# Kernel optimization log

Measured on AMD Instinct MI355X. Metric: run time of the kernel, lower is better.

The kernel has to match this reference:

```python
import jax, jax.numpy as jnp
import numpy as np

B, S, D, H = 2, 2048, 1024, 16
DK = D // H


def setup_inputs() -> dict:
    key = jax.random.key(0)
    ks = jax.random.split(key, 8)
    Q = jax.random.normal(ks[0], (B, S, D), dtype=jnp.float32)
    K = jax.random.normal(ks[1], (B, S, D), dtype=jnp.float32)
    V = jax.random.normal(ks[2], (B, S, D), dtype=jnp.float32)
    # causal mask (1 = keep), broadcastable to [B, H, S, S]
    mask = jnp.tril(jnp.ones((S, S), dtype=bool))[None, None, :, :]
    # xavier_uniform for [D, D]: bound = sqrt(6 / (D + D))
    bound = float(np.sqrt(6.0 / (D + D)))
    def xavier(k):
        return jax.random.uniform(k, (D, D), jnp.float32, -bound, bound)
    Wq, Wk, Wv, Wo = xavier(ks[3]), xavier(ks[4]), xavier(ks[5]), xavier(ks[6])
    bq = jnp.zeros((D,), jnp.float32)
    bk = jnp.zeros((D,), jnp.float32)
    bv = jnp.zeros((D,), jnp.float32)
    bo = jnp.zeros((D,), jnp.float32)
    return {"Q": Q, "K": K, "V": V, "mask": mask,
            "Wq": Wq, "bq": bq, "Wk": Wk, "bk": bk,
            "Wv": Wv, "bv": bv, "Wo": Wo, "bo": bo}


def _split_heads(x):
    # [B, S, D] -> [B, H, S, DK]
    b, s, _ = x.shape
    return x.reshape(b, s, H, DK).transpose(0, 2, 1, 3)


def reference(Q, K, V, mask, Wq, bq, Wk, bk, Wv, bv, Wo, bo):
    # linear projections (torch Linear: x @ W.T + b)
    q = _split_heads(Q @ Wq.T + bq)  # [B, H, S, DK]
    k = _split_heads(K @ Wk.T + bk)
    v = _split_heads(V @ Wv.T + bv)
    scale = 1.0 / jnp.sqrt(jnp.asarray(DK, q.dtype))
    scores = jnp.einsum('bhqd,bhkd->bhqk', q, k) * scale  # [B, H, S, S]
    scores = jnp.where(mask, scores, jnp.asarray(-1e9, scores.dtype))
    attn = jax.nn.softmax(scores, axis=-1)
    ctx = jnp.einsum('bhqk,bhkd->bhqd', attn, v)  # [B, H, S, DK]
    ctx = ctx.transpose(0, 2, 1, 3).reshape(Q.shape[0], Q.shape[1], D)
    out = ctx @ Wo.T + bo  # dropout is identity in eval mode
    return out, attn
```

## Files before the change

### kernel.cpp

```cpp
#include <hip/hip_runtime.h>
#include <hip/hip_bf16.h>

#define B_  2
#define S_  2048
#define D_  1024
#define H_  16
#define DK_ 64
#define M_  (B_*S_)
#define NT_ (S_/64)
#define NE_ (B_*S_*D_)
#define NW_ (D_*D_)

typedef __attribute__((ext_vector_type(8))) short short8;
typedef __attribute__((ext_vector_type(4))) float f32x4;

static __device__ __forceinline__ unsigned short f2bf(float f) {
    union { float f; unsigned u; } v; v.f = f;
    unsigned r = (v.u + 0x7fffu + ((v.u >> 16) & 1u)) >> 16;
    return (unsigned short)r;
}

static __device__ __forceinline__ void gload16(const void* g, void* l) {
    __builtin_amdgcn_global_load_lds((const __attribute__((address_space(1))) void*)g,
                                     (__attribute__((address_space(3))) void*)l, 16, 0, 0);
}

__global__ __launch_bounds__(256) void conv7(const float* __restrict__ q,  const float* __restrict__ k,
                                             const float* __restrict__ v,  const float* __restrict__ wq,
                                             const float* __restrict__ wk, const float* __restrict__ wv,
                                             const float* __restrict__ wo, unsigned short* __restrict__ ws)
{
    const float* src[7] = {q, k, v, wq, wk, wv, wo};
    const int    n4[7]  = {NE_/4, NE_/4, NE_/4, NW_/4, NW_/4, NW_/4, NW_/4};
    size_t off = 0;
    #pragma unroll
    for (int seg = 0; seg < 7; ++seg) {
        unsigned short* dst = ws + off;
        for (int i = blockIdx.x*256 + threadIdx.x; i < n4[seg]; i += gridDim.x*256) {
            float4 x = ((const float4*)src[seg])[i];
            union { unsigned short u[4]; unsigned long long ll; } cv;
            cv.u[0]=f2bf(x.x); cv.u[1]=f2bf(x.y); cv.u[2]=f2bf(x.z); cv.u[3]=f2bf(x.w);
            ((unsigned long long*)dst)[i] = cv.ll;
        }
        off += (size_t)n4[seg]*4;
    }
}

__global__ __launch_bounds__(256) void gemm_bt(const unsigned short* __restrict__ A,
                                               const unsigned short* __restrict__ Bt,
                                               const float* __restrict__ bias,
                                               void* __restrict__ outv, int out_mode)
{
    __shared__ unsigned short as_[128][64];
    __shared__ unsigned short bs_[64][64];

    const int tid  = threadIdx.x;
    const int wave = tid >> 6, lane = tid & 63;
    const int lq   = lane & 15, quad = lane >> 4;
    const int m0   = blockIdx.y * 128, n0 = blockIdx.x * 64;
    const int wm   = (wave >> 1) * 64, wn = (wave & 1) * 32;

    f32x4 acc[4][2] = {};

    for (int k0 = 0; k0 < D_; k0 += 64) {
        __syncthreads();
        #pragma unroll
        for (int i = 0; i < 4; ++i) {
            const int p = tid + i*256, row = p >> 3, c = (p & 7) ^ (row & 7);
            gload16(A + (size_t)(m0+row)*D_ + k0 + c*8,
                    (char*)as_ + (size_t)(wave*64 + i*256)*16);
        }
        #pragma unroll
        for (int i = 0; i < 2; ++i) {
            const int p = tid + i*256, row = p >> 3, c = (p & 7) ^ (row & 7);
            gload16(Bt + (size_t)(n0+row)*D_ + k0 + c*8,
                    (char*)bs_ + (size_t)(wave*64 + i*256)*16);
        }
        __syncthreads();

        #pragma unroll
        for (int kk = 0; kk < 2; ++kk) {
            short8 a[4], b[2];
            #pragma unroll
            for (int i = 0; i < 4; ++i) {
                const int row = wm + i*16 + lq;
                a[i] = *(const short8*)((const char*)as_ + row*128 + (((kk*4+quad) ^ (row&7))*16));
            }
            #pragma unroll
            for (int j = 0; j < 2; ++j) {
                const int row = wn + j*16 + lq;
                b[j] = *(const short8*)((const char*)bs_ + row*128 + (((kk*4+quad) ^ (row&7))*16));
            }
            #pragma unroll
            for (int i = 0; i < 4; ++i)
                #pragma unroll
                for (int j = 0; j < 2; ++j)
                    acc[i][j] = __builtin_amdgcn_mfma_f32_16x16x32_bf16(a[i], b[j], acc[i][j], 0, 0, 0);
        }
    }

    float bcol[2];
    #pragma unroll
    for (int j = 0; j < 2; ++j) bcol[j] = bias[n0 + wn + j*16 + lq];

    if (out_mode == 0) {
        float* out = (float*)outv;
        #pragma unroll
        for (int i = 0; i < 4; ++i)
            #pragma unroll
            for (int j = 0; j < 2; ++j) {
                const int col = n0 + wn + j*16 + lq;
                #pragma unroll
                for (int r = 0; r < 4; ++r) {
                    const int m = m0 + wm + i*16 + quad*4 + r;
                    out[(size_t)m*D_ + col] = acc[i][j][r] + bcol[j];
                }
            }
    } else {
        unsigned short* out = (unsigned short*)outv;
        #pragma unroll
        for (int i = 0; i < 4; ++i)
            #pragma unroll
            for (int j = 0; j < 2; ++j) {
                const int col = n0 + wn + j*16 + lq;
                const int h = col >> 6, dk = col & 63;
                #pragma unroll
                for (int r = 0; r < 4; ++r) {
                    const int m  = m0 + wm + i*16 + quad*4 + r;
                    const int bb = m >> 11, s = m & (S_-1);
                    out[(((size_t)(bb*H_ + h))*S_ + s)*DK_ + dk] = f2bf(acc[i][j][r] + bcol[j]);
                }
            }
    }
}

__global__ __launch_bounds__(256) void transpose_v(const unsigned short* __restrict__ vp,
                                                   unsigned short* __restrict__ vt)
{
    __shared__ unsigned short ts[64][72];
    const int tid = threadIdx.x;
    const int s0  = blockIdx.x * 64;
    const size_t bh = (size_t)blockIdx.z * H_ + blockIdx.y;
    const unsigned short* src = vp + (bh * S_ + s0) * DK_;
    #pragma unroll
    for (int i = 0; i < 2; ++i) {
        int idx = tid + i*256;
        *(short8*)&ts[idx >> 3][(idx & 7)*8] = *(const short8*)(src + idx*8);
    }
    __syncthreads();
    unsigned short* dst = vt + bh * DK_ * S_;
    #pragma unroll
    for (int i = 0; i < 2; ++i) {
        int idx = tid + i*256;
        int dk = idx >> 3, c = idx & 7;
        union { unsigned short u[8]; short8 v; } pk;
        #pragma unroll
        for (int j = 0; j < 8; ++j) pk.u[j] = ts[c*8 + j][dk];
        *(short8*)(dst + (size_t)dk*S_ + s0 + c*8) = pk.v;
    }
}

__global__ __launch_bounds__(256) void attn_mfma(const unsigned short* __restrict__ q,
                                                 const unsigned short* __restrict__ k,
                                                 const unsigned short* __restrict__ vt,
                                                 float* __restrict__ attn,
                                                 unsigned short* __restrict__ ctx)
{
    __shared__ unsigned short qs[2][64][64];
    __shared__ unsigned short ks[64][64];
    __shared__ unsigned short vts[64][64];
    __shared__ unsigned short es[4][16][72];

    const int tid  = threadIdx.x;
    const int wave = tid >> 6, lane = tid & 63;
    const int lq   = lane & 15, quad = lane >> 4;

    const int g = blockIdx.x;
    const int xcd = g & 7, i5 = g >> 3;
    const int x = i5 >> 2;
    const int bhid = xcd + 8*(i5 & 3);
    const int h = bhid & (H_-1), b = bhid >> 4;

    const int itA = x, itB = NT_-1 - x;
    const size_t bh = (size_t)(b*H_ + h);
    const unsigned short* kb  = k  + bh*S_*DK_;
    const unsigned short* vtb = vt + bh*(size_t)DK_*S_;
    const unsigned short* qbA = q + (bh*S_ + (size_t)itA*64) * DK_;
    const unsigned short* qbB = q + (bh*S_ + (size_t)itB*64) * DK_;
    float* attn_bA = attn + bh*(size_t)S_*S_ + (size_t)itA*64*S_;
    float* attn_bB = attn + bh*(size_t)S_*S_ + (size_t)itB*64*S_;

    #pragma unroll
    for (int t = 0; t < 2; ++t) {
        const unsigned short* qb = t ? qbB : qbA;
        #pragma unroll
        for (int i = 0; i < 2; ++i) {
            const int p = tid + i*256, row = p >> 3, c = (p & 7) ^ (row & 7);
            gload16(qb + (size_t)row*DK_ + c*8,
                    (char*)&qs[t][0][0] + (size_t)(wave*64 + i*256)*16);
        }
    }
    __syncthreads();

    const int wr0  = wave*16;
    const int rgA0 = itA*64 + wr0 + quad*4;
    const int rgB0 = itB*64 + wr0 + quad*4;

    short8 aA0, aA1, aB0, aB1;
    {
        const int row = wr0 + lq;
        const int s0 = ((quad)     ^ (row & 7)) * 16;
        const int s1 = ((4 + quad) ^ (row & 7)) * 16;
        aA0 = *(const short8*)((const char*)&qs[0][row][0] + s0);
        aA1 = *(const short8*)((const char*)&qs[0][row][0] + s1);
        aB0 = *(const short8*)((const char*)&qs[1][row][0] + s0);
        aB1 = *(const short8*)((const char*)&qs[1][row][0] + s1);
    }

    float rsA[4] = {0.f,0.f,0.f,0.f}, rsB[4] = {0.f,0.f,0.f,0.f};
    for (int jt = 0; jt <= itB; ++jt) {
        __syncthreads();
        #pragma unroll
        for (int i = 0; i < 2; ++i) {
            const int p = tid + i*256, row = p >> 3, c = (p & 7) ^ (row & 7);
            gload16(kb + ((size_t)jt*64 + row)*DK_ + c*8,
                    (char*)&ks[0][0] + (size_t)(wave*64 + i*256)*16);
        }
        __syncthreads();
        const int actA = (jt <= itA);
        #pragma unroll
        for (int j = 0; j < 4; ++j) {
            const int krow = j*16 + lq;
            const int s0 = ((quad)     ^ (krow & 7)) * 16;
            const int s1 = ((4 + quad) ^ (krow & 7)) * 16;
            const short8 b0 = *(const short8*)((const char*)&ks[krow][0] + s0);
            const short8 b1 = *(const short8*)((const char*)&ks[krow][0] + s1);
            const int cg = jt*64 + j*16 + lq;
            {
                f32x4 s = {};
                s = __builtin_amdgcn_mfma_f32_16x16x32_bf16(aB0, b0, s, 0, 0, 0);
                s = __builtin_amdgcn_mfma_f32_16x16x32_bf16(aB1, b1, s, 0, 0, 0);
                #pragma unroll
                for (int r = 0; r < 4; ++r)
                    if (cg <= rgB0 + r) rsB[r] += __expf(s[r]*0.125f);
            }
            if (actA) {
                f32x4 s = {};
                s = __builtin_amdgcn_mfma_f32_16x16x32_bf16(aA0, b0, s, 0, 0, 0);
                s = __builtin_amdgcn_mfma_f32_16x16x32_bf16(aA1, b1, s, 0, 0, 0);
                #pragma unroll
                for (int r = 0; r < 4; ++r)
                    if (cg <= rgA0 + r) rsA[r] += __expf(s[r]*0.125f);
            }
        }
    }
    #pragma unroll
    for (int m = 1; m < 16; m <<= 1)
        #pragma unroll
        for (int r = 0; r < 4; ++r) {
            rsA[r] += __shfl_xor(rsA[r], m, 64);
            rsB[r] += __shfl_xor(rsB[r], m, 64);
        }
    float invA[4], invB[4];
    #pragma unroll
    for (int r = 0; r < 4; ++r) { invA[r] = 1.0f/rsA[r]; invB[r] = 1.0f/rsB[r]; }

    f32x4 cA[4] = {}, cB[4] = {};
    for (int jt = 0; jt <= itB; ++jt) {
        __syncthreads();
        #pragma unroll
        for (int i = 0; i < 2; ++i) {
            const int p = tid + i*256, row = p >> 3, c = (p & 7) ^ (row & 7);
            gload16(kb + ((size_t)jt*64 + row)*DK_ + c*8,
                    (char*)&ks[0][0]  + (size_t)(wave*64 + i*256)*16);
            gload16(vtb + (size_t)row*S_ + jt*64 + c*8,
                    (char*)&vts[0][0] + (size_t)(wave*64 + i*256)*16);
        }
        __syncthreads();
        const int actA = (jt <= itA);

        #pragma unroll
        for (int j = 0; j < 4; ++j) {
            const int krow = j*16 + lq;
            const int s0 = ((quad)     ^ (krow & 7)) * 16;
            const int s1 = ((4 + quad) ^ (krow & 7)) * 16;
            const short8 b0 = *(const short8*)((const char*)&ks[krow][0] + s0);
            const short8 b1 = *(const short8*)((const char*)&ks[krow][0] + s1);
            const int cg = jt*64 + j*16 + lq;
            f32x4 s = {};
            s = __builtin_amdgcn_mfma_f32_16x16x32_bf16(aB0, b0, s, 0, 0, 0);
            s = __builtin_amdgcn_mfma_f32_16x16x32_bf16(aB1, b1, s, 0, 0, 0);
            #pragma unroll
            for (int r = 0; r < 4; ++r) {
                const float e = (cg <= rgB0 + r) ? __expf(s[r]*0.125f)*invB[r] : 0.f;
                attn_bB[(size_t)(wr0 + quad*4 + r)*S_ + cg] = e;
                es[wave][quad*4 + r][j*16 + lq] = f2bf(e);
            }
        }
        {
            const short8 p0 = *(const short8*)&es[wave][lq][quad*8];
            const short8 p1 = *(const short8*)&es[wave][lq][32 + quad*8];
            #pragma unroll
            for (int j = 0; j < 4; ++j) {
                const int vrow = j*16 + lq;
                const int s0 = ((quad)     ^ (vrow & 7)) * 16;
                const int s1 = ((4 + quad) ^ (vrow & 7)) * 16;
                cB[j] = __builtin_amdgcn_mfma_f32_16x16x32_bf16(
                    p0, *(const short8*)((const char*)&vts[vrow][0] + s0), cB[j], 0, 0, 0);
                cB[j] = __builtin_amdgcn_mfma_f32_16x16x32_bf16(
                    p1, *(const short8*)((const char*)&vts[vrow][0] + s1), cB[j], 0, 0, 0);
            }
        }

        if (actA) {
            #pragma unroll
            for (int j = 0; j < 4; ++j) {
                const int krow = j*16 + lq;
                const int s0 = ((quad)     ^ (krow & 7)) * 16;
                const int s1 = ((4 + quad) ^ (krow & 7)) * 16;
                const short8 b0 = *(const short8*)((const char*)&ks[krow][0] + s0);
                const short8 b1 = *(const short8*)((const char*)&ks[krow][0] + s1);
                const int cg = jt*64 + j*16 + lq;
                f32x4 s = {};
                s = __builtin_amdgcn_mfma_f32_16x16x32_bf16(aA0, b0, s, 0, 0, 0);
                s = __builtin_amdgcn_mfma_f32_16x16x32_bf16(aA1, b1, s, 0, 0, 0);
                #pragma unroll
                for (int r = 0; r < 4; ++r) {
                    const float e = (cg <= rgA0 + r) ? __expf(s[r]*0.125f)*invA[r] : 0.f;
                    attn_bA[(size_t)(wr0 + quad*4 + r)*S_ + cg] = e;
                    es[wave][quad*4 + r][j*16 + lq] = f2bf(e);
                }
            }
            const short8 p0 = *(const short8*)&es[wave][lq][quad*8];
            const short8 p1 = *(const short8*)&es[wave][lq][32 + quad*8];
            #pragma unroll
            for (int j = 0; j < 4; ++j) {
                const int vrow = j*16 + lq;
                const int s0 = ((quad)     ^ (vrow & 7)) * 16;
                const int s1 = ((4 + quad) ^ (vrow & 7)) * 16;
                cA[j] = __builtin_amdgcn_mfma_f32_16x16x32_bf16(
                    p0, *(const short8*)((const char*)&vts[vrow][0] + s0), cA[j], 0, 0, 0);
                cA[j] = __builtin_amdgcn_mfma_f32_16x16x32_bf16(
                    p1, *(const short8*)((const char*)&vts[vrow][0] + s1), cA[j], 0, 0, 0);
            }
        }
    }

    #pragma unroll
    for (int j = 0; j < 4; ++j) {
        const int dk = j*16 + lq;
        #pragma unroll
        for (int r = 0; r < 4; ++r) {
            const int sA = itA*64 + wr0 + quad*4 + r;
            const int sB = itB*64 + wr0 + quad*4 + r;
            ctx[((size_t)b*S_ + sA)*D_ + h*DK_ + dk] = f2bf(cA[j][r]);
            ctx[((size_t)b*S_ + sB)*D_ + h*DK_ + dk] = f2bf(cB[j][r]);
        }
    }

    const float4 z4 = make_float4(0.f, 0.f, 0.f, 0.f);
    {
        const int zc0 = (itA+1)*64;
        float* rowp = attn_bA + (size_t)(tid >> 2)*S_;
        for (int c = zc0 + (tid & 3)*4; c < S_; c += 16) *(float4*)&rowp[c] = z4;
    }
    {
        const int zc0 = (itB+1)*64;
        if (zc0 < S_) {
            float* rowp = attn_bB + (size_t)(tid >> 2)*S_;
            for (int c = zc0 + (tid & 3)*4; c < S_; c += 16) *(float4*)&rowp[c] = z4;
        }
    }
}

extern "C" void kernel_launch(void* const* d_in, const int* in_sizes, int n_in,
                              void* d_out, int out_size, void* d_ws, size_t ws_size,
                              hipStream_t stream)
{
    const float* Q  = (const float*)d_in[0];
    const float* K  = (const float*)d_in[1];
    const float* V  = (const float*)d_in[2];
    const float* Wq = (const float*)d_in[4];
    const float* bq = (const float*)d_in[5];
    const float* Wk = (const float*)d_in[6];
    const float* bk = (const float*)d_in[7];
    const float* Wv = (const float*)d_in[8];
    const float* bv = (const float*)d_in[9];
    const float* Wo = (const float*)d_in[10];
    const float* bo = (const float*)d_in[11];

    float* out  = (float*)d_out;
    float* attn = out + (size_t)B_*S_*D_;

    unsigned short* ws = (unsigned short*)d_ws;
    const size_t R  = (size_t)NE_;
    const size_t W1 = (size_t)NW_;
    unsigned short* Qb  = ws;
    unsigned short* Kb  = ws + R;
    unsigned short* Vb  = ws + 2*R;
    unsigned short* Wqb = ws + 3*R;
    unsigned short* Wkb = Wqb + W1;
    unsigned short* Wvb = Wkb + W1;
    unsigned short* Wob = Wvb + W1;
    unsigned short* qp  = Wob + W1;
    unsigned short* kp  = qp + R;
    unsigned short* vp  = kp + R;
    unsigned short* vtw = vp + R;
    unsigned short* ctx = vtw + R;

    conv7<<<2048, 256, 0, stream>>>(Q, K, V, Wq, Wk, Wv, Wo, ws);

    dim3 ggrid(D_/64, M_/128);
    gemm_bt<<<ggrid, 256, 0, stream>>>(Qb, Wqb, bq, qp, 1);
    gemm_bt<<<ggrid, 256, 0, stream>>>(Kb, Wkb, bk, kp, 1);
    gemm_bt<<<ggrid, 256, 0, stream>>>(Vb, Wvb, bv, vp, 1);
    transpose_v<<<dim3(S_/64, H_, B_), 256, 0, stream>>>(vp, vtw);
    attn_mfma<<<(NT_/2)*H_*B_, 256, 0, stream>>>(qp, kp, vtw, attn, ctx);
    gemm_bt<<<ggrid, 256, 0, stream>>>(ctx, Wob, bo, out, 0);
}
```

Measured before the change: 806.2 us.

## Double-buffer GEMM and attention tiles, batch QKV GEMMs, split attention across 8 waves

```diff
diff --git a/kernel.cpp b/kernel.cpp
--- a/kernel.cpp
+++ b/kernel.cpp
@@ -46,50 +46,62 @@
     }
 }
 
-__global__ __launch_bounds__(256) void gemm_bt(const unsigned short* __restrict__ A,
-                                               const unsigned short* __restrict__ Bt,
-                                               const float* __restrict__ bias,
+__global__ __launch_bounds__(256) void gemm_bt(const unsigned short* __restrict__ A0,
+                                               const unsigned short* __restrict__ W0,
+                                               const float* __restrict__ b0,
+                                               const float* __restrict__ b1,
+                                               const float* __restrict__ b2,
                                                void* __restrict__ outv, int out_mode)
 {
-    __shared__ unsigned short as_[128][64];
-    __shared__ unsigned short bs_[64][64];
+    __shared__ unsigned short as2[2][128][64];
+    __shared__ unsigned short bs2[2][64][64];
 
     const int tid  = threadIdx.x;
-    const int wave = tid >> 6, lane = tid & 63;
+    const int wave = tid >> 6;
+    const int lane = tid & 63;
     const int lq   = lane & 15, quad = lane >> 4;
+    const int z    = blockIdx.z;
     const int m0   = blockIdx.y * 128, n0 = blockIdx.x * 64;
     const int wm   = (wave >> 1) * 64, wn = (wave & 1) * 32;
 
+    const unsigned short* A  = A0 + (size_t)z * NE_;
+    const unsigned short* Bt = W0 + (size_t)z * NW_;
+    const float* bias = (z == 0) ? b0 : (z == 1 ? b1 : b2);
+
     f32x4 acc[4][2] = {};
 
-    for (int k0 = 0; k0 < D_; k0 += 64) {
-        __syncthreads();
+    auto STAGE = [&](int k0, int buf) {
         #pragma unroll
         for (int i = 0; i < 4; ++i) {
             const int p = tid + i*256, row = p >> 3, c = (p & 7) ^ (row & 7);
             gload16(A + (size_t)(m0+row)*D_ + k0 + c*8,
-                    (char*)as_ + (size_t)(wave*64 + i*256)*16);
+                    (char*)&as2[buf][0][0] + (size_t)(wave*64 + i*256)*16);
         }
         #pragma unroll
         for (int i = 0; i < 2; ++i) {
             const int p = tid + i*256, row = p >> 3, c = (p & 7) ^ (row & 7);
             gload16(Bt + (size_t)(n0+row)*D_ + k0 + c*8,
-                    (char*)bs_ + (size_t)(wave*64 + i*256)*16);
-        }
-        __syncthreads();
-
+                    (char*)&bs2[buf][0][0] + (size_t)(wave*64 + i*256)*16);
+        }
+    };
+
+    STAGE(0, 0);
+    __syncthreads();
+    int cur = 0;
+    for (int k0 = 0; k0 < D_; k0 += 64) {
+        if (k0 + 64 < D_) STAGE(k0 + 64, cur ^ 1);
         #pragma unroll
         for (int kk = 0; kk < 2; ++kk) {
             short8 a[4], b[2];
             #pragma unroll
             for (int i = 0; i < 4; ++i) {
                 const int row = wm + i*16 + lq;
-                a[i] = *(const short8*)((const char*)as_ + row*128 + (((kk*4+quad) ^ (row&7))*16));
+                a[i] = *(const short8*)((const char*)&as2[cur][0][0] + row*128 + (((kk*4+quad) ^ (row&7))*16));
             }
             #pragma unroll
             for (int j = 0; j < 2; ++j) {
                 const int row = wn + j*16 + lq;
-                b[j] = *(const short8*)((const char*)bs_ + row*128 + (((kk*4+quad) ^ (row&7))*16));
+                b[j] = *(const short8*)((const char*)&bs2[cur][0][0] + row*128 + (((kk*4+quad) ^ (row&7))*16));
             }
             #pragma unroll
             for (int i = 0; i < 4; ++i)
@@ -97,6 +109,8 @@
                 for (int j = 0; j < 2; ++j)
                     acc[i][j] = __builtin_amdgcn_mfma_f32_16x16x32_bf16(a[i], b[j], acc[i][j], 0, 0, 0);
         }
+        __syncthreads();
+        cur ^= 1;
     }
 
     float bcol[2];
@@ -117,7 +131,7 @@
                 }
             }
     } else {
-        unsigned short* out = (unsigned short*)outv;
+        unsigned short* out = (unsigned short*)outv + (size_t)z * NE_;
         #pragma unroll
         for (int i = 0; i < 4; ++i)
             #pragma unroll
@@ -160,20 +174,21 @@
     }
 }
 
-__global__ __launch_bounds__(256) void attn_mfma(const unsigned short* __restrict__ q,
+__global__ __launch_bounds__(512) void attn_mfma(const unsigned short* __restrict__ q,
                                                  const unsigned short* __restrict__ k,
                                                  const unsigned short* __restrict__ vt,
                                                  float* __restrict__ attn,
                                                  unsigned short* __restrict__ ctx)
 {
-    __shared__ unsigned short qs[2][64][64];
-    __shared__ unsigned short ks[64][64];
-    __shared__ unsigned short vts[64][64];
-    __shared__ unsigned short es[4][16][72];
+    __shared__ unsigned short qs_es[9216];
+    __shared__ unsigned short ks2[2][64][64];
+    __shared__ unsigned short vts2[2][64][64];
 
     const int tid  = threadIdx.x;
     const int wave = tid >> 6, lane = tid & 63;
     const int lq   = lane & 15, quad = lane >> 4;
+    const int ts   = wave >> 2;
+    const int wr0  = (wave & 3) * 16;
 
     const int g = blockIdx.x;
     const int xcd = g & 7, i5 = g >> 3;
@@ -182,168 +197,132 @@
     const int h = bhid & (H_-1), b = bhid >> 4;
 
     const int itA = x, itB = NT_-1 - x;
+    const int itM = ts ? itB : itA;
     const size_t bh = (size_t)(b*H_ + h);
     const unsigned short* kb  = k  + bh*S_*DK_;
     const unsigned short* vtb = vt + bh*(size_t)DK_*S_;
     const unsigned short* qbA = q + (bh*S_ + (size_t)itA*64) * DK_;
     const unsigned short* qbB = q + (bh*S_ + (size_t)itB*64) * DK_;
-    float* attn_bA = attn + bh*(size_t)S_*S_ + (size_t)itA*64*S_;
-    float* attn_bB = attn + bh*(size_t)S_*S_ + (size_t)itB*64*S_;
-
-    #pragma unroll
-    for (int t = 0; t < 2; ++t) {
-        const unsigned short* qb = t ? qbB : qbA;
-        #pragma unroll
-        for (int i = 0; i < 2; ++i) {
-            const int p = tid + i*256, row = p >> 3, c = (p & 7) ^ (row & 7);
-            gload16(qb + (size_t)row*DK_ + c*8,
-                    (char*)&qs[t][0][0] + (size_t)(wave*64 + i*256)*16);
-        }
+    float* attn_bM = attn + bh*(size_t)S_*S_ + (size_t)itM*64*S_;
+
+    {
+        const int row = tid >> 3, c = (tid & 7) ^ (row & 7);
+        gload16(qbA + (size_t)row*DK_ + c*8, (char*)qs_es + tid*16);
+        gload16(qbB + (size_t)row*DK_ + c*8, (char*)qs_es + 8192 + tid*16);
+        gload16(kb  + (size_t)row*DK_ + c*8, (char*)&ks2[0][0][0] + tid*16);
     }
     __syncthreads();
 
-    const int wr0  = wave*16;
-    const int rgA0 = itA*64 + wr0 + quad*4;
-    const int rgB0 = itB*64 + wr0 + quad*4;
-
-    short8 aA0, aA1, aB0, aB1;
+    short8 aT0, aT1;
     {
         const int row = wr0 + lq;
-        const int s0 = ((quad)     ^ (row & 7)) * 16;
-        const int s1 = ((4 + quad) ^ (row & 7)) * 16;
-        aA0 = *(const short8*)((const char*)&qs[0][row][0] + s0);
-        aA1 = *(const short8*)((const char*)&qs[0][row][0] + s1);
-        aB0 = *(const short8*)((const char*)&qs[1][row][0] + s0);
-        aB1 = *(const short8*)((const char*)&qs[1][row][0] + s1);
-    }
-
-    float rsA[4] = {0.f,0.f,0.f,0.f}, rsB[4] = {0.f,0.f,0.f,0.f};
+        const char* qrow = (const char*)qs_es + ts*8192 + row*128;
+        aT0 = *(const short8*)(qrow + ((quad     ^ (row & 7)) * 16));
+        aT1 = *(const short8*)(qrow + (((4+quad) ^ (row & 7)) * 16));
+    }
+    const int rg0 = itM*64 + wr0 + quad*4;
+
+    float rs[4] = {0.f, 0.f, 0.f, 0.f};
+    int cur = 0;
     for (int jt = 0; jt <= itB; ++jt) {
+        if (jt < itB) {
+            const int row = tid >> 3, c = (tid & 7) ^ (row & 7);
+            gload16(kb + ((size_t)(jt+1)*64 + row)*DK_ + c*8,
+                    (char*)&ks2[cur^1][0][0] + tid*16);
+        }
+        if (jt <= itM) {
+            f32x4 sa[4];
+            __builtin_amdgcn_s_setprio(1);
+            #pragma unroll
+            for (int j = 0; j < 4; ++j) {
+                const int krow = j*16 + lq;
+                const char* kp8 = (const char*)&ks2[cur][0][0] + krow*128;
+                const short8 b0 = *(const short8*)(kp8 + ((quad     ^ (krow&7)) * 16));
+                const short8 b1 = *(const short8*)(kp8 + (((4+quad) ^ (krow&7)) * 16));
+                f32x4 s = {};
+                s = __builtin_amdgcn_mfma_f32_16x16x32_bf16(aT0, b0, s, 0, 0, 0);
+                s = __builtin_amdgcn_mfma_f32_16x16x32_bf16(aT1, b1, s, 0, 0, 0);
+                sa[j] = s;
+            }
+            __builtin_amdgcn_s_setprio(0);
+            #pragma unroll
+            for (int j = 0; j < 4; ++j) {
+                const int cg = jt*64 + j*16 + lq;
+                #pragma unroll
+                for (int r = 0; r < 4; ++r)
+                    if (cg <= rg0 + r) rs[r] += __expf(sa[j][r]*0.125f);
+            }
+        }
         __syncthreads();
-        #pragma unroll
-        for (int i = 0; i < 2; ++i) {
-            const int p = tid + i*256, row = p >> 3, c = (p & 7) ^ (row & 7);
-            gload16(kb + ((size_t)jt*64 + row)*DK_ + c*8,
-                    (char*)&ks[0][0] + (size_t)(wave*64 + i*256)*16);
+        cur ^= 1;
+    }
+
+    {
+        const int row = tid >> 3, c = (tid & 7) ^ (row & 7);
+        gload16(kb  + (size_t)row*DK_ + c*8, (char*)&ks2[0][0][0]  + tid*16);
+        gload16(vtb + (size_t)row*S_  + c*8, (char*)&vts2[0][0][0] + tid*16);
+    }
+    #pragma unroll
+    for (int m = 1; m < 16; m <<= 1)
+        #pragma unroll
+        for (int r = 0; r < 4; ++r) rs[r] += __shfl_xor(rs[r], m, 64);
+    float inv[4];
+    #pragma unroll
+    for (int r = 0; r < 4; ++r) inv[r] = 1.0f / rs[r];
+    __syncthreads();
+
+    unsigned short* es = qs_es;
+    f32x4 cacc[4] = {};
+    cur = 0;
+    for (int jt = 0; jt <= itB; ++jt) {
+        if (jt < itB) {
+            const int row = tid >> 3, c = (tid & 7) ^ (row & 7);
+            gload16(kb  + ((size_t)(jt+1)*64 + row)*DK_ + c*8,
+                    (char*)&ks2[cur^1][0][0]  + tid*16);
+            gload16(vtb + (size_t)row*S_ + (jt+1)*64 + c*8,
+                    (char*)&vts2[cur^1][0][0] + tid*16);
+        }
+        if (jt <= itM) {
+            f32x4 sa[4];
+            __builtin_amdgcn_s_setprio(1);
+            #pragma unroll
+            for (int j = 0; j < 4; ++j) {
+                const int krow = j*16 + lq;
+                const char* kp8 = (const char*)&ks2[cur][0][0] + krow*128;
+                const short8 b0 = *(const short8*)(kp8 + ((quad     ^ (krow&7)) * 16));
+                const short8 b1 = *(const short8*)(kp8 + (((4+quad) ^ (krow&7)) * 16));
+                f32x4 s = {};
+                s = __builtin_amdgcn_mfma_f32_16x16x32_bf16(aT0, b0, s, 0, 0, 0);
+                s = __builtin_amdgcn_mfma_f32_16x16x32_bf16(aT1, b1, s, 0, 0, 0);
+                sa[j] = s;
+            }
+            __builtin_amdgcn_s_setprio(0);
+            #pragma unroll
+            for (int j = 0; j < 4; ++j) {
+                const int cg = jt*64 + j*16 + lq;
+                #pragma unroll
+                for (int r = 0; r < 4; ++r) {
+                    const float e = (cg <= rg0 + r) ? __expf(sa[j][r]*0.125f)*inv[r] : 0.f;
+                    attn_bM[(size_t)(wr0 + quad*4 + r)*S_ + cg] = e;
+                    es[wave*1152 + (quad*4 + r)*72 + j*16 + lq] = f2bf(e);
+                }
+            }
+            const short8 p0 = *(const short8*)&es[wave*1152 + lq*72 + quad*8];
+            const short8 p1 = *(const short8*)&es[wave*1152 + lq*72 + 32 + quad*8];
+            __builtin_amdgcn_s_setprio(1);
+            #pragma unroll
+            for (int j = 0; j < 4; ++j) {
+                const int vrow = j*16 + lq;
+                const char* vp8 = (const char*)&vts2[cur][0][0] + vrow*128;
+                cacc[j] = __builtin_amdgcn_mfma_f32_16x16x32_bf16(
+                    p0, *(const short8*)(vp8 + ((quad     ^ (vrow&7)) * 16)), cacc[j], 0, 0, 0);
+                cacc[j] = __builtin_amdgcn_mfma_f32_16x16x32_bf16(
+                    p1, *(const short8*)(vp8 + (((4+quad) ^ (vrow&7)) * 16)), cacc[j], 0, 0, 0);
+            }
+            __builtin_amdgcn_s_setprio(0);
         }
         __syncthreads();
-        const int actA = (jt <= itA);
-        #pragma unroll
-        for (int j = 0; j < 4; ++j) {
-            const int krow = j*16 + lq;
-            const int s0 = ((quad)     ^ (krow & 7)) * 16;
-            const int s1 = ((4 + quad) ^ (krow & 7)) * 16;
-            const short8 b0 = *(const short8*)((const char*)&ks[krow][0] + s0);
-            const short8 b1 = *(const short8*)((const char*)&ks[krow][0] + s1);
-            const int cg = jt*64 + j*16 + lq;
-            {
-                f32x4 s = {};
-                s = __builtin_amdgcn_mfma_f32_16x16x32_bf16(aB0, b0, s, 0, 0, 0);
-                s = __builtin_amdgcn_mfma_f32_16x16x32_bf16(aB1, b1, s, 0, 0, 0);
-                #pragma unroll
-                for (int r = 0; r < 4; ++r)
-                    if (cg <= rgB0 + r) rsB[r] += __expf(s[r]*0.125f);
-            }
-            if (actA) {
-                f32x4 s = {};
-                s = __builtin_amdgcn_mfma_f32_16x16x32_bf16(aA0, b0, s, 0, 0, 0);
-                s = __builtin_amdgcn_mfma_f32_16x16x32_bf16(aA1, b1, s, 0, 0, 0);
-                #pragma unroll
-                for (int r = 0; r < 4; ++r)
-                    if (cg <= rgA0 + r) rsA[r] += __expf(s[r]*0.125f);
-            }
-        }
-    }
-    #pragma unroll
-    for (int m = 1; m < 16; m <<= 1)
-        #pragma unroll
-        for (int r = 0; r < 4; ++r) {
-            rsA[r] += __shfl_xor(rsA[r], m, 64);
-            rsB[r] += __shfl_xor(rsB[r], m, 64);
-        }
-    float invA[4], invB[4];
-    #pragma unroll
-    for (int r = 0; r < 4; ++r) { invA[r] = 1.0f/rsA[r]; invB[r] = 1.0f/rsB[r]; }
-
-    f32x4 cA[4] = {}, cB[4] = {};
-    for (int jt = 0; jt <= itB; ++jt) {
-        __syncthreads();
-        #pragma unroll
-        for (int i = 0; i < 2; ++i) {
-            const int p = tid + i*256, row = p >> 3, c = (p & 7) ^ (row & 7);
-            gload16(kb + ((size_t)jt*64 + row)*DK_ + c*8,
-                    (char*)&ks[0][0]  + (size_t)(wave*64 + i*256)*16);
-            gload16(vtb + (size_t)row*S_ + jt*64 + c*8,
-                    (char*)&vts[0][0] + (size_t)(wave*64 + i*256)*16);
-        }
-        __syncthreads();
-        const int actA = (jt <= itA);
-
-        #pragma unroll
-        for (int j = 0; j < 4; ++j) {
-            const int krow = j*16 + lq;
-            const int s0 = ((quad)     ^ (krow & 7)) * 16;
-            const int s1 = ((4 + quad) ^ (krow & 7)) * 16;
-            const short8 b0 = *(const short8*)((const char*)&ks[krow][0] + s0);
-            const short8 b1 = *(const short8*)((const char*)&ks[krow][0] + s1);
-            const int cg = jt*64 + j*16 + lq;
-            f32x4 s = {};
-            s = __builtin_amdgcn_mfma_f32_16x16x32_bf16(aB0, b0, s, 0, 0, 0);
-            s = __builtin_amdgcn_mfma_f32_16x16x32_bf16(aB1, b1, s, 0, 0, 0);
-            #pragma unroll
-            for (int r = 0; r < 4; ++r) {
-                const float e = (cg <= rgB0 + r) ? __expf(s[r]*0.125f)*invB[r] : 0.f;
-                attn_bB[(size_t)(wr0 + quad*4 + r)*S_ + cg] = e;
-                es[wave][quad*4 + r][j*16 + lq] = f2bf(e);
-            }
-        }
-        {
-            const short8 p0 = *(const short8*)&es[wave][lq][quad*8];
-            const short8 p1 = *(const short8*)&es[wave][lq][32 + quad*8];
-            #pragma unroll
-            for (int j = 0; j < 4; ++j) {
-                const int vrow = j*16 + lq;
-                const int s0 = ((quad)     ^ (vrow & 7)) * 16;
-                const int s1 = ((4 + quad) ^ (vrow & 7)) * 16;
-                cB[j] = __builtin_amdgcn_mfma_f32_16x16x32_bf16(
-                    p0, *(const short8*)((const char*)&vts[vrow][0] + s0), cB[j], 0, 0, 0);
-                cB[j] = __builtin_amdgcn_mfma_f32_16x16x32_bf16(
-                    p1, *(const short8*)((const char*)&vts[vrow][0] + s1), cB[j], 0, 0, 0);
-            }
-        }
-
-        if (actA) {
-            #pragma unroll
-            for (int j = 0; j < 4; ++j) {
-                const int krow = j*16 + lq;
-                const int s0 = ((quad)     ^ (krow & 7)) * 16;
-                const int s1 = ((4 + quad) ^ (krow & 7)) * 16;
-                const short8 b0 = *(const short8*)((const char*)&ks[krow][0] + s0);
-                const short8 b1 = *(const short8*)((const char*)&ks[krow][0] + s1);
-                const int cg = jt*64 + j*16 + lq;
-                f32x4 s = {};
-                s = __builtin_amdgcn_mfma_f32_16x16x32_bf16(aA0, b0, s, 0, 0, 0);
-                s = __builtin_amdgcn_mfma_f32_16x16x32_bf16(aA1, b1, s, 0, 0, 0);
-                #pragma unroll
-                for (int r = 0; r < 4; ++r) {
-                    const float e = (cg <= rgA0 + r) ? __expf(s[r]*0.125f)*invA[r] : 0.f;
-                    attn_bA[(size_t)(wr0 + quad*4 + r)*S_ + cg] = e;
-                    es[wave][quad*4 + r][j*16 + lq] = f2bf(e);
-                }
-            }
-            const short8 p0 = *(const short8*)&es[wave][lq][quad*8];
-            const short8 p1 = *(const short8*)&es[wave][lq][32 + quad*8];
-            #pragma unroll
-            for (int j = 0; j < 4; ++j) {
-                const int vrow = j*16 + lq;
-                const int s0 = ((quad)     ^ (vrow & 7)) * 16;
-                const int s1 = ((4 + quad) ^ (vrow & 7)) * 16;
-                cA[j] = __builtin_amdgcn_mfma_f32_16x16x32_bf16(
-                    p0, *(const short8*)((const char*)&vts[vrow][0] + s0), cA[j], 0, 0, 0);
-                cA[j] = __builtin_amdgcn_mfma_f32_16x16x32_bf16(
-                    p1, *(const short8*)((const char*)&vts[vrow][0] + s1), cA[j], 0, 0, 0);
-            }
-        }
+        cur ^= 1;
     }
 
     #pragma unroll
@@ -351,24 +330,18 @@
         const int dk = j*16 + lq;
         #pragma unroll
         for (int r = 0; r < 4; ++r) {
-            const int sA = itA*64 + wr0 + quad*4 + r;
-            const int sB = itB*64 + wr0 + quad*4 + r;
-            ctx[((size_t)b*S_ + sA)*D_ + h*DK_ + dk] = f2bf(cA[j][r]);
-            ctx[((size_t)b*S_ + sB)*D_ + h*DK_ + dk] = f2bf(cB[j][r]);
+            const int srow = itM*64 + wr0 + quad*4 + r;
+            ctx[((size_t)b*S_ + srow)*D_ + h*DK_ + dk] = f2bf(cacc[j][r]);
         }
     }
 
     const float4 z4 = make_float4(0.f, 0.f, 0.f, 0.f);
     {
-        const int zc0 = (itA+1)*64;
-        float* rowp = attn_bA + (size_t)(tid >> 2)*S_;
-        for (int c = zc0 + (tid & 3)*4; c < S_; c += 16) *(float4*)&rowp[c] = z4;
-    }
-    {
-        const int zc0 = (itB+1)*64;
+        const int t = tid & 255;
+        const int zc0 = (itM + 1) * 64;
         if (zc0 < S_) {
-            float* rowp = attn_bB + (size_t)(tid >> 2)*S_;
-            for (int c = zc0 + (tid & 3)*4; c < S_; c += 16) *(float4*)&rowp[c] = z4;
+            float* rowp = attn_bM + (size_t)(t >> 2)*S_;
+            for (int c = zc0 + (t & 3)*4; c < S_; c += 16) *(float4*)&rowp[c] = z4;
         }
     }
 }
@@ -396,25 +369,18 @@
     const size_t R  = (size_t)NE_;
     const size_t W1 = (size_t)NW_;
     unsigned short* Qb  = ws;
-    unsigned short* Kb  = ws + R;
-    unsigned short* Vb  = ws + 2*R;
     unsigned short* Wqb = ws + 3*R;
-    unsigned short* Wkb = Wqb + W1;
-    unsigned short* Wvb = Wkb + W1;
-    unsigned short* Wob = Wvb + W1;
+    unsigned short* Wob = Wqb + 3*W1;
     unsigned short* qp  = Wob + W1;
     unsigned short* kp  = qp + R;
-    unsigned short* vp  = kp + R;
-    unsigned short* vtw = vp + R;
+    unsigned short* vp  = qp + 2*R;
+    unsigned short* vtw = qp + 3*R;
     unsigned short* ctx = vtw + R;
 
     conv7<<<2048, 256, 0, stream>>>(Q, K, V, Wq, Wk, Wv, Wo, ws);
 
-    dim3 ggrid(D_/64, M_/128);
-    gemm_bt<<<ggrid, 256, 0, stream>>>(Qb, Wqb, bq, qp, 1);
-    gemm_bt<<<ggrid, 256, 0, stream>>>(Kb, Wkb, bk, kp, 1);
-    gemm_bt<<<ggrid, 256, 0, stream>>>(Vb, Wvb, bv, vp, 1);
+    gemm_bt<<<dim3(D_/64, M_/128, 3), 256, 0, stream>>>(Qb, Wqb, bq, bk, bv, qp, 1);
     transpose_v<<<dim3(S_/64, H_, B_), 256, 0, stream>>>(vp, vtw);
-    attn_mfma<<<(NT_/2)*H_*B_, 256, 0, stream>>>(qp, kp, vtw, attn, ctx);
-    gemm_bt<<<ggrid, 256, 0, stream>>>(ctx, Wob, bo, out, 0);
-}
+    attn_mfma<<<(NT_/2)*H_*B_, 512, 0, stream>>>(qp, kp, vtw, attn, ctx);
+    gemm_bt<<<dim3(D_/64, M_/128, 1), 256, 0, stream>>>(ctx, Wob, bo, bo, bo, out, 0);
+}
```

Result: no change. 816.7 us (+1.3%).

## Batch QKV projections into one launch with 128x128 tiles and fused V transpose

Applied to the files above, without the earlier changes.

```diff
diff --git a/kernel.cpp b/kernel.cpp
--- a/kernel.cpp
+++ b/kernel.cpp
@@ -46,21 +46,40 @@
     }
 }
 
-__global__ __launch_bounds__(256) void gemm_bt(const unsigned short* __restrict__ A,
-                                               const unsigned short* __restrict__ Bt,
-                                               const float* __restrict__ bias,
-                                               void* __restrict__ outv, int out_mode)
+__global__ __launch_bounds__(256) void gemm_bt(const unsigned short* __restrict__ A0,
+                                               const unsigned short* __restrict__ W0,
+                                               const float* __restrict__ b0,
+                                               const float* __restrict__ b1,
+                                               const float* __restrict__ b2,
+                                               void* __restrict__ outv,
+                                               void* __restrict__ outv2,
+                                               int out_mode)
 {
     __shared__ unsigned short as_[128][64];
-    __shared__ unsigned short bs_[64][64];
+    __shared__ unsigned short bs_[128][64];
 
     const int tid  = threadIdx.x;
-    const int wave = tid >> 6, lane = tid & 63;
+    const int wave = tid >> 6;
+    const int lane = tid & 63;
     const int lq   = lane & 15, quad = lane >> 4;
-    const int m0   = blockIdx.y * 128, n0 = blockIdx.x * 64;
-    const int wm   = (wave >> 1) * 64, wn = (wave & 1) * 32;
-
-    f32x4 acc[4][2] = {};
+
+    const int g     = blockIdx.x;
+    const int xcd   = g & 7;
+    const int local = g >> 3;
+    const int m_loc = local & 3;
+    const int rest  = local >> 2;
+    const int n_t   = rest & 7;
+    const int z     = rest >> 3;
+
+    const int m0 = (xcd*4 + m_loc) * 128;
+    const int n0 = n_t * 128;
+    const int wm = (wave >> 1) * 64, wn = (wave & 1) * 64;
+
+    const unsigned short* A  = A0 + (size_t)z * NE_;
+    const unsigned short* Bt = W0 + (size_t)z * NW_;
+    const float* bias = (z == 0) ? b0 : (z == 1 ? b1 : b2);
+
+    f32x4 acc[4][4] = {};
 
     for (int k0 = 0; k0 < D_; k0 += 64) {
         __syncthreads();
@@ -71,7 +90,7 @@
                     (char*)as_ + (size_t)(wave*64 + i*256)*16);
         }
         #pragma unroll
-        for (int i = 0; i < 2; ++i) {
+        for (int i = 0; i < 4; ++i) {
             const int p = tid + i*256, row = p >> 3, c = (p & 7) ^ (row & 7);
             gload16(Bt + (size_t)(n0+row)*D_ + k0 + c*8,
                     (char*)bs_ + (size_t)(wave*64 + i*256)*16);
@@ -80,35 +99,35 @@
 
         #pragma unroll
         for (int kk = 0; kk < 2; ++kk) {
-            short8 a[4], b[2];
+            short8 a[4], b[4];
             #pragma unroll
             for (int i = 0; i < 4; ++i) {
                 const int row = wm + i*16 + lq;
                 a[i] = *(const short8*)((const char*)as_ + row*128 + (((kk*4+quad) ^ (row&7))*16));
             }
             #pragma unroll
-            for (int j = 0; j < 2; ++j) {
+            for (int j = 0; j < 4; ++j) {
                 const int row = wn + j*16 + lq;
                 b[j] = *(const short8*)((const char*)bs_ + row*128 + (((kk*4+quad) ^ (row&7))*16));
             }
             #pragma unroll
             for (int i = 0; i < 4; ++i)
                 #pragma unroll
-                for (int j = 0; j < 2; ++j)
+                for (int j = 0; j < 4; ++j)
                     acc[i][j] = __builtin_amdgcn_mfma_f32_16x16x32_bf16(a[i], b[j], acc[i][j], 0, 0, 0);
         }
     }
 
-    float bcol[2];
-    #pragma unroll
-    for (int j = 0; j < 2; ++j) bcol[j] = bias[n0 + wn + j*16 + lq];
+    float bcol[4];
+    #pragma unroll
+    for (int j = 0; j < 4; ++j) bcol[j] = bias[n0 + wn + j*16 + lq];
 
     if (out_mode == 0) {
         float* out = (float*)outv;
         #pragma unroll
         for (int i = 0; i < 4; ++i)
             #pragma unroll
-            for (int j = 0; j < 2; ++j) {
+            for (int j = 0; j < 4; ++j) {
                 const int col = n0 + wn + j*16 + lq;
                 #pragma unroll
                 for (int r = 0; r < 4; ++r) {
@@ -116,12 +135,12 @@
                     out[(size_t)m*D_ + col] = acc[i][j][r] + bcol[j];
                 }
             }
-    } else {
-        unsigned short* out = (unsigned short*)outv;
+    } else if (z < 2) {
+        unsigned short* out = (unsigned short*)outv + (size_t)z * NE_;
         #pragma unroll
         for (int i = 0; i < 4; ++i)
             #pragma unroll
-            for (int j = 0; j < 2; ++j) {
+            for (int j = 0; j < 4; ++j) {
                 const int col = n0 + wn + j*16 + lq;
                 const int h = col >> 6, dk = col & 63;
                 #pragma unroll
@@ -131,32 +150,21 @@
                     out[(((size_t)(bb*H_ + h))*S_ + s)*DK_ + dk] = f2bf(acc[i][j][r] + bcol[j]);
                 }
             }
-    }
-}
-
-__global__ __launch_bounds__(256) void transpose_v(const unsigned short* __restrict__ vp,
-                                                   unsigned short* __restrict__ vt)
-{
-    __shared__ unsigned short ts[64][72];
-    const int tid = threadIdx.x;
-    const int s0  = blockIdx.x * 64;
-    const size_t bh = (size_t)blockIdx.z * H_ + blockIdx.y;
-    const unsigned short* src = vp + (bh * S_ + s0) * DK_;
-    #pragma unroll
-    for (int i = 0; i < 2; ++i) {
-        int idx = tid + i*256;
-        *(short8*)&ts[idx >> 3][(idx & 7)*8] = *(const short8*)(src + idx*8);
-    }
-    __syncthreads();
-    unsigned short* dst = vt + bh * DK_ * S_;
-    #pragma unroll
-    for (int i = 0; i < 2; ++i) {
-        int idx = tid + i*256;
-        int dk = idx >> 3, c = idx & 7;
-        union { unsigned short u[8]; short8 v; } pk;
-        #pragma unroll
-        for (int j = 0; j < 8; ++j) pk.u[j] = ts[c*8 + j][dk];
-        *(short8*)(dst + (size_t)dk*S_ + s0 + c*8) = pk.v;
+    } else {
+        unsigned short* out = (unsigned short*)outv2;
+        #pragma unroll
+        for (int i = 0; i < 4; ++i)
+            #pragma unroll
+            for (int j = 0; j < 4; ++j) {
+                const int col = n0 + wn + j*16 + lq;
+                const int h = col >> 6, dk = col & 63;
+                const int m  = m0 + wm + i*16 + quad*4;
+                const int bb = m >> 11, s = m & (S_-1);
+                union { unsigned short u[4]; unsigned long long ll; } pk;
+                #pragma unroll
+                for (int r = 0; r < 4; ++r) pk.u[r] = f2bf(acc[i][j][r] + bcol[j]);
+                *(unsigned long long*)&out[(((size_t)(bb*H_ + h))*DK_ + dk)*S_ + s] = pk.ll;
+            }
     }
 }
 
@@ -272,7 +280,7 @@
         for (int i = 0; i < 2; ++i) {
             const int p = tid + i*256, row = p >> 3, c = (p & 7) ^ (row & 7);
             gload16(kb + ((size_t)jt*64 + row)*DK_ + c*8,
-                    (char*)&ks[0][0]  + (size_t)(wave*64 + i*256)*16);
+                    (char*)&ks[0][0] + (size_t)(wave*64 + i*256)*16);
             gload16(vtb + (size_t)row*S_ + jt*64 + c*8,
                     (char*)&vts[0][0] + (size_t)(wave*64 + i*256)*16);
         }
@@ -396,25 +404,16 @@
     const size_t R  = (size_t)NE_;
     const size_t W1 = (size_t)NW_;
     unsigned short* Qb  = ws;
-    unsigned short* Kb  = ws + R;
-    unsigned short* Vb  = ws + 2*R;
     unsigned short* Wqb = ws + 3*R;
-    unsigned short* Wkb = Wqb + W1;
-    unsigned short* Wvb = Wkb + W1;
-    unsigned short* Wob = Wvb + W1;
+    unsigned short* Wob = Wqb + 3*W1;
     unsigned short* qp  = Wob + W1;
     unsigned short* kp  = qp + R;
-    unsigned short* vp  = kp + R;
-    unsigned short* vtw = vp + R;
+    unsigned short* vtw = qp + 2*R;
     unsigned short* ctx = vtw + R;
 
     conv7<<<2048, 256, 0, stream>>>(Q, K, V, Wq, Wk, Wv, Wo, ws);
 
-    dim3 ggrid(D_/64, M_/128);
-    gemm_bt<<<ggrid, 256, 0, stream>>>(Qb, Wqb, bq, qp, 1);
-    gemm_bt<<<ggrid, 256, 0, stream>>>(Kb, Wkb, bk, kp, 1);
-    gemm_bt<<<ggrid, 256, 0, stream>>>(Vb, Wvb, bv, vp, 1);
-    transpose_v<<<dim3(S_/64, H_, B_), 256, 0, stream>>>(vp, vtw);
+    gemm_bt<<<768, 256, 0, stream>>>(Qb, Wqb, bq, bk, bv, qp, vtw, 1);
     attn_mfma<<<(NT_/2)*H_*B_, 256, 0, stream>>>(qp, kp, vtw, attn, ctx);
-    gemm_bt<<<ggrid, 256, 0, stream>>>(ctx, Wob, bo, out, 0);
-}
+    gemm_bt<<<256, 256, 0, stream>>>(ctx, Wob, bo, bo, bo, out, nullptr, 0);
+}
```

Measured after the change: 804.2 us. No clear change (-0.2%).
